# Kernel tuning notes

Measured on AMD Instinct MI355X. Metric: run time of the kernel, lower is better.

The kernel has to match this reference:

```python
import jax, jax.numpy as jnp
import numpy as np

IMG, P, CIN, D, K, L, H, FF, B = 512, 32, 3, 256, 8192, 6, 8, 1024, 32
GRID = IMG // P  # 16
DH = D // H
EPS = 1e-5


def _ln(x, w, b):
    m = x.mean(-1, keepdims=True)
    v = ((x - m) ** 2).mean(-1, keepdims=True)
    return (x - m) / jnp.sqrt(v + EPS) * w + b


def _mha(x, wqkv, bqkv, wo, bo):
    # x: (S, Bt, D) -- axis 0 is the attention axis (torch batch_first=False quirk)
    S, Bt, _ = x.shape
    qkv = x @ wqkv.T + bqkv
    q, k, v = jnp.split(qkv, 3, axis=-1)
    q = q.reshape(S, Bt, H, DH)
    k = k.reshape(S, Bt, H, DH)
    v = v.reshape(S, Bt, H, DH)
    scores = jnp.einsum('sbhd,tbhd->bhst', q, k) / jnp.sqrt(jnp.float32(DH))
    attn = jax.nn.softmax(scores, axis=-1)
    o = jnp.einsum('bhst,tbhd->sbhd', attn, v).reshape(S, Bt, D)
    return o @ wo.T + bo


def _conv_t(x, w, b, stride=2, pad=1):
    # w uses torch ConvTranspose2d layout (Cin, Cout, kH, kW)
    kH = w.shape[2]
    wf = jnp.flip(w, (2, 3)).transpose(1, 0, 2, 3)  # -> (Cout, Cin, kH, kW)
    y = jax.lax.conv_general_dilated(
        x, wf, window_strides=(1, 1),
        padding=[(kH - 1 - pad, kH - 1 - pad)] * 2,
        lhs_dilation=(stride, stride),
        dimension_numbers=('NCHW', 'OIHW', 'NCHW'))
    return y + b[None, :, None, None]


def _forward(x, patch_w, patch_b, qkv_w, qkv_b, out_w, out_b, ln1_w, ln1_b,
             ln2_w, ln2_b, ff1_w, ff1_b, ff2_w, ff2_b, lnf_w, lnf_b, codebook,
             dec_w0, dec_b0, dec_w1, dec_b1, dec_w2, dec_b2, dec_w3, dec_b3):
    # patch embedding: conv stride=patch -> (B, D, G, G) -> (B, N, D)
    h = jax.lax.conv_general_dilated(
        x, patch_w, (P, P), 'VALID',
        dimension_numbers=('NCHW', 'OIHW', 'NCHW')) + patch_b[None, :, None, None]
    h = h.reshape(h.shape[0], D, -1).transpose(0, 2, 1)  # (B, N, D)
    # torch TransformerEncoderLayer default batch_first=False: attention runs
    # over axis 0 (image batch); faithfully replicated here. Post-norm, eval
    # mode (dropout=identity), exact gelu.
    for i in range(L):
        a = _mha(h, qkv_w[i], qkv_b[i], out_w[i], out_b[i])
        h = _ln(h + a, ln1_w[i], ln1_b[i])
        f = jax.nn.gelu(h @ ff1_w[i].T + ff1_b[i], approximate=False) @ ff2_w[i].T + ff2_b[i]
        h = _ln(h + f, ln2_w[i], ln2_b[i])
    h = _ln(h, lnf_w, lnf_b)
    # vector quantization: squared-distance argmin over codebook
    flat = h.reshape(-1, D)  # (B*N, D)
    d = ((flat ** 2).sum(-1, keepdims=True)
         - 2.0 * flat @ codebook.T
         + (codebook ** 2).sum(-1))  # (B*N, K)
    idx = jnp.argmin(d, axis=1)
    q = codebook[idx].reshape(h.shape)
    e_loss = jnp.mean((jax.lax.stop_gradient(q) - h) ** 2)
    q_loss = jnp.mean((q - jax.lax.stop_gradient(h)) ** 2)
    vq_loss = q_loss + 0.25 * e_loss
    q = h + jax.lax.stop_gradient(q - h)  # straight-through
    q = q.transpose(0, 2, 1).reshape(x.shape[0], D, GRID, GRID)
    y = jax.nn.relu(_conv_t(q, dec_w0, dec_b0))
    y = jax.nn.relu(_conv_t(y, dec_w1, dec_b1))
    y = jax.nn.relu(_conv_t(y, dec_w2, dec_b2))
    x_hat = jax.nn.sigmoid(_conv_t(y, dec_w3, dec_b3))
    return x_hat, vq_loss


def setup_inputs() -> dict:
    key = jax.random.key(0)
    ks = iter(jax.random.split(key, 64))
    nrm = lambda shape, s=0.02: jax.random.normal(next(ks), shape, jnp.float32) * s
    f32 = jnp.float32
    return {
        'x': jax.random.normal(next(ks), (B, CIN, IMG, IMG), f32),
        'patch_w': nrm((D, CIN, P, P)),
        'patch_b': jnp.zeros((D,), f32),
        'qkv_w': nrm((L, 3 * D, D)),
        'qkv_b': jnp.zeros((L, 3 * D), f32),
        'out_w': nrm((L, D, D)),
        'out_b': jnp.zeros((L, D), f32),
        'ln1_w': jnp.ones((L, D), f32),
        'ln1_b': jnp.zeros((L, D), f32),
        'ln2_w': jnp.ones((L, D), f32),
        'ln2_b': jnp.zeros((L, D), f32),
        'ff1_w': nrm((L, FF, D)),
        'ff1_b': jnp.zeros((L, FF), f32),
        'ff2_w': nrm((L, D, FF)),
        'ff2_b': jnp.zeros((L, D), f32),
        'lnf_w': jnp.ones((D,), f32),
        'lnf_b': jnp.zeros((D,), f32),
        'codebook': jax.random.uniform(next(ks), (K, D), f32, -1.0 / K, 1.0 / K),
        'dec_w0': nrm((D, 256, 4, 4)),
        'dec_b0': jnp.zeros((256,), f32),
        'dec_w1': nrm((256, 128, 4, 4)),
        'dec_b1': jnp.zeros((128,), f32),
        'dec_w2': nrm((128, 64, 4, 4)),
        'dec_b2': jnp.zeros((64,), f32),
        'dec_w3': nrm((64, CIN, 4, 4)),
        'dec_b3': jnp.zeros((CIN,), f32),
    }


def reference(x, patch_w, patch_b, qkv_w, qkv_b, out_w, out_b, ln1_w, ln1_b,
              ln2_w, ln2_b, ff1_w, ff1_b, ff2_w, ff2_b, lnf_w, lnf_b, codebook,
              dec_w0, dec_b0, dec_w1, dec_b1, dec_w2, dec_b2, dec_w3, dec_b3):
    return _forward(x, patch_w, patch_b, qkv_w, qkv_b, out_w, out_b, ln1_w,
                    ln1_b, ln2_w, ln2_b, ff1_w, ff1_b, ff2_w, ff2_b, lnf_w,
                    lnf_b, codebook, dec_w0, dec_b0, dec_w1, dec_b1, dec_w2,
                    dec_b2, dec_w3, dec_b3)
```

## Files before the change

### kernel.cpp

```cpp
#include <hip/hip_runtime.h>
#include <hip/hip_bf16.h>
#include <math.h>

typedef __hip_bfloat16 bf16;
typedef unsigned int u32;
typedef unsigned long long u64;
using short8 = __attribute__((ext_vector_type(8))) short;
using f32x4  = __attribute__((ext_vector_type(4))) float;

__device__ __forceinline__ float b2f(bf16 v){ return __bfloat162float(v); }
__device__ __forceinline__ bf16  f2b(float v){ return __float2bfloat16(v); }
__device__ __forceinline__ float plo(u32 u){ return __uint_as_float(u << 16); }
__device__ __forceinline__ float phi(u32 u){ return __uint_as_float(u & 0xffff0000u); }

__device__ __forceinline__ void gld16(const void* g, void* l)
{
  __builtin_amdgcn_global_load_lds(
      (const __attribute__((address_space(1))) u32*)g,
      (__attribute__((address_space(3))) u32*)l, 16, 0, 0);
}

__global__ void k_detect(const u32* probe, int* flag)
{
  if (threadIdx.x == 0 && blockIdx.x == 0)
    *flag = (*probe == 0x3F800000u) ? 0 : 1;
}

struct PPack { const void* s[25]; u32 off[26]; };
__global__ __launch_bounds__(256) void k_convall(PPack pp, bf16* P, const int* flag)
{
  const u32 i = blockIdx.x * 256 + threadIdx.x;
  if (i >= pp.off[25]) return;
  int lo = 0, hi = 25;
  while (hi - lo > 1) { const int mid = (lo + hi) >> 1; if (i >= pp.off[mid]) lo = mid; else hi = mid; }
  const u32 j = i - pp.off[lo];
  P[i] = *flag ? ((const bf16*)pp.s[lo])[j] : f2b(((const float*)pp.s[lo])[j]);
}

__global__ __launch_bounds__(256) void k_zborder(bf16* buf, int Hp, int C, int nimg)
{
  const int per = 4 * Hp - 4;
  const int c8 = C >> 3;
  const int total = nimg * per * c8;
  const int i = blockIdx.x * 256 + threadIdx.x;
  if (i >= total) return;
  const int ch8 = i % c8;
  const int pb = i / c8;
  const int img = pb / per;
  const int b = pb - img * per;
  int y, x;
  if (b < Hp) { y = 0; x = b; }
  else if (b < 2 * Hp) { y = Hp - 1; x = b - Hp; }
  else {
    const int r = b - 2 * Hp;
    const int side = r / (Hp - 2);
    y = 1 + r - side * (Hp - 2);
    x = side ? (Hp - 1) : 0;
  }
  uint4 z = {0, 0, 0, 0};
  *reinterpret_cast<uint4*>(buf + (((size_t)img * Hp + y) * Hp + x) * C + ch8 * 8) = z;
}

__global__ __launch_bounds__(128) void k_im2col(const void* x, bf16* A, const int* flag)
{
  const int m = blockIdx.y;
  const int k8 = blockIdx.x * 128 + threadIdx.x;
  const int k = k8 * 8;
  const int b = m >> 8, n = m & 255;
  const int gy = n >> 4, gx = n & 15;
  const int c = k >> 10, r = (k >> 5) & 31, pp = k & 31;
  const size_t src = (((size_t)(b * 3 + c) * 512) + gy * 32 + r) * 512 + gx * 32 + pp;
  bf16 ov[8];
  if (*flag) {
    const bf16* xp = (const bf16*)x + src;
    #pragma unroll
    for (int i = 0; i < 8; ++i) ov[i] = xp[i];
  } else {
    const float4 v0 = *reinterpret_cast<const float4*>((const float*)x + src);
    const float4 v1 = *reinterpret_cast<const float4*>((const float*)x + src + 4);
    ov[0]=f2b(v0.x); ov[1]=f2b(v0.y); ov[2]=f2b(v0.z); ov[3]=f2b(v0.w);
    ov[4]=f2b(v1.x); ov[5]=f2b(v1.y); ov[6]=f2b(v1.z); ov[7]=f2b(v1.w);
  }
  *reinterpret_cast<uint4*>(A + (size_t)m * 3072 + k) = *reinterpret_cast<const uint4*>(ov);
}

template<int EPI, int FM, int BN, bool DB>
__global__ __launch_bounds__(256, 2) void gemm_t(
    const bf16* __restrict__ A, const bf16* __restrict__ Bw,
    const bf16* __restrict__ bias, const bf16* res, bf16* C,
    const float* __restrict__ cnorm, u64* __restrict__ ku,
    int M, int N, int K, int Kc)
{
  constexpr int BM = FM * 32;
  constexpr int FN = BN / 32;
  __shared__ alignas(16) bf16 As[DB ? 2 : 1][BM * 64];
  __shared__ alignas(16) bf16 Bs[DB ? 2 : 1][BN * 64];
  const int tid = threadIdx.x;
  const int bn = blockIdx.x * BN, bm = blockIdx.y * BM;
  const int z = blockIdx.z;
  const int kb = z * Kc;
  const int l = tid & 63, w = tid >> 6;
  const int wm = w >> 1, wn = w & 1;
  const int lg = l >> 4, lr = l & 15;
  const int sr8 = l >> 3;
  const int sch = (l & 7) ^ sr8;
  f32x4 acc[FM][FN];
  #pragma unroll
  for (int fm = 0; fm < FM; ++fm)
    #pragma unroll
    for (int fn = 0; fn < FN; ++fn) acc[fm][fn] = (f32x4){0.f, 0.f, 0.f, 0.f};

  auto stage = [&](int bb, int k0) {
    char* ab = (char*)As[bb];
    char* bp = (char*)Bs[bb];
    #pragma unroll
    for (int it = 0; it < FM; ++it) {
      const int r = w * 8 + it * 32 + sr8;
      gld16(A + (size_t)(bm + r) * K + k0 + sch * 8, ab + w * 1024 + it * 4096);
    }
    #pragma unroll
    for (int it = 0; it < BN / 32; ++it) {
      const int r = w * 8 + it * 32 + sr8;
      gld16(Bw + (size_t)(bn + r) * K + k0 + sch * 8, bp + w * 1024 + it * 4096);
    }
  };
  auto compute = [&](int bb) {
    const char* ab = (const char*)As[bb];
    const char* bp = (const char*)Bs[bb];
    #pragma unroll
    for (int ks = 0; ks < 2; ++ks) {
      short8 af[FM], bfr[FN];
      #pragma unroll
      for (int fm = 0; fm < FM; ++fm) {
        const int r = wm * (FM * 16) + fm * 16 + lr;
        af[fm] = *reinterpret_cast<const short8*>(ab + r * 128 + (((lg + ks * 4) ^ (r & 7)) * 16));
      }
      #pragma unroll
      for (int fn = 0; fn < FN; ++fn) {
        const int r = wn * (BN / 2) + fn * 16 + lr;
        bfr[fn] = *reinterpret_cast<const short8*>(bp + r * 128 + (((lg + ks * 4) ^ (r & 7)) * 16));
      }
      #pragma unroll
      for (int fm = 0; fm < FM; ++fm)
        #pragma unroll
        for (int fn = 0; fn < FN; ++fn)
          acc[fm][fn] = __builtin_amdgcn_mfma_f32_16x16x32_bf16(af[fm], bfr[fn], acc[fm][fn], 0, 0, 0);
    }
  };

  const int nt = Kc >> 6;
  if (DB) {
    stage(0, kb);
    __syncthreads();
    for (int t = 0; t < nt; ++t) {
      const int cur = t & 1;
      if (t + 1 < nt) stage(cur ^ 1, kb + ((t + 1) << 6));
      compute(cur);
      __syncthreads();
    }
  } else {
    for (int t = 0; t < nt; ++t) {
      if (t) __syncthreads();
      stage(0, kb + (t << 6));
      __syncthreads();
      compute(0);
    }
  }

  if (EPI == 3) {
    __shared__ u64 skey[BM][2];
    float cn[FN];
    #pragma unroll
    for (int fn = 0; fn < FN; ++fn) cn[fn] = cnorm[bn + wn * (BN / 2) + fn * 16 + lr];
    #pragma unroll
    for (int fm = 0; fm < FM; ++fm) {
      #pragma unroll
      for (int r = 0; r < 4; ++r) {
        u64 best = ~0ull;
        #pragma unroll
        for (int fn = 0; fn < FN; ++fn) {
          const int col = bn + wn * (BN / 2) + fn * 16 + lr;
          const float d = cn[fn] - 2.0f * acc[fm][fn][r];
          u32 u = __float_as_uint(d);
          u = (u & 0x80000000u) ? ~u : (u | 0x80000000u);
          const u64 key = ((u64)u << 32) | (u32)col;
          best = key < best ? key : best;
        }
        #pragma unroll
        for (int mk = 1; mk < 16; mk <<= 1) {
          const u64 o = __shfl_xor(best, mk, 64);
          best = o < best ? o : best;
        }
        if (lr == 0) skey[wm * (FM * 16) + fm * 16 + lg * 4 + r][wn] = best;
      }
    }
    __syncthreads();
    if (tid < BM) {
      const u64 a = skey[tid][0], b = skey[tid][1];
      ku[(size_t)blockIdx.x * M + bm + tid] = a < b ? a : b;
    }
  } else if (EPI == 4) {
    #pragma unroll
    for (int fm = 0; fm < FM; ++fm) {
      const int m0 = bm + wm * (FM * 16) + fm * 16 + lg * 4;
      #pragma unroll
      for (int fn = 0; fn < FN; ++fn) {
        const int n = bn + wn * (BN / 2) + fn * 16 + lr;
        #pragma unroll
        for (int r = 0; r < 4; ++r)
          C[((size_t)z * M + m0 + r) * N + n] = f2b(acc[fm][fn][r]);
      }
    }
  } else {
    #pragma unroll
    for (int fm = 0; fm < FM; ++fm) {
      const int m0 = bm + wm * (FM * 16) + fm * 16 + lg * 4;
      #pragma unroll
      for (int fn = 0; fn < FN; ++fn) {
        const int n = bn + wn * (BN / 2) + fn * 16 + lr;
        const float bs = b2f(bias[n]);
        #pragma unroll
        for (int r = 0; r < 4; ++r) {
          float v = acc[fm][fn][r] + bs;
          if (EPI == 1) v = 0.5f * v * (1.0f + erff(v * 0.70710678118654752f));
          if (EPI == 2) v += b2f(res[(size_t)(m0 + r) * N + n]);
          C[(size_t)(m0 + r) * N + n] = f2b(v);
        }
      }
    }
  }
}

__global__ __launch_bounds__(256, 1) void k_fat1(
    bf16* __restrict__ hbuf,
    const bf16* __restrict__ Wqkv, const bf16* __restrict__ Bqkv,
    const bf16* __restrict__ Wo, const bf16* __restrict__ Bo,
    const bf16* __restrict__ lw, const bf16* __restrict__ lb)
{
  __shared__ alignas(16) bf16 hs[32 * 256];
  __shared__ alignas(16) bf16 ao[32 * 256];
  __shared__ alignas(16) bf16 astage[128 * 64];
  __shared__ bf16 att[3 * 9216];
  __shared__ float ps[32][33];
  __shared__ float rs[32];
  __shared__ float psum[32][4], psq[32][4];
  __shared__ float mstat[32], istat[32];

  const int bt = blockIdx.x;
  const int tid = threadIdx.x;
  const int l = tid & 63, w = tid >> 6;
  const int lg = l >> 4, lr = l & 15;
  const int sr8 = l >> 3;
  const int sch = (l & 7) ^ sr8;
  char* hsb = (char*)hs;
  char* aob = (char*)ao;
  char* asb = (char*)astage;

  #pragma unroll
  for (int call = 0; call < 4; ++call) {
    const int id = call * 256 + tid;
    const int s = id >> 5, within = id & 31;
    const int grp = within >> 3, c = within & 7;
    gld16(hbuf + (size_t)(s * 256 + bt) * 256 + grp * 64 + ((c ^ (s & 7)) * 8),
          hsb + call * 4096 + w * 1024);
  }

  for (int at = 0; at < 6; ++at) {
    f32x4 acc[2][2];
    #pragma unroll
    for (int fm = 0; fm < 2; ++fm)
      #pragma unroll
      for (int fn = 0; fn < 2; ++fn) acc[fm][fn] = (f32x4){0.f, 0.f, 0.f, 0.f};
    for (int kst = 0; kst < 4; ++kst) {
      __syncthreads();
      #pragma unroll
      for (int it = 0; it < 4; ++it) {
        const int r = w * 8 + it * 32 + sr8;
        gld16(Wqkv + (size_t)(at * 128 + r) * 256 + kst * 64 + sch * 8,
              asb + w * 1024 + it * 4096);
      }
      __syncthreads();
      #pragma unroll
      for (int ks = 0; ks < 2; ++ks) {
        short8 af[2], bfr[2];
        #pragma unroll
        for (int fm = 0; fm < 2; ++fm) {
          const int r = w * 32 + fm * 16 + lr;
          af[fm] = *reinterpret_cast<const short8*>(asb + r * 128 + (((lg + ks * 4) ^ (r & 7)) * 16));
        }
        #pragma unroll
        for (int fn = 0; fn < 2; ++fn) {
          const int sr = fn * 16 + lr;
          bfr[fn] = *reinterpret_cast<const short8*>(hsb + sr * 512 + kst * 128 + (((lg + ks * 4) ^ (sr & 7)) * 16));
        }
        #pragma unroll
        for (int fm = 0; fm < 2; ++fm)
          #pragma unroll
          for (int fn = 0; fn < 2; ++fn)
            acc[fm][fn] = __builtin_amdgcn_mfma_f32_16x16x32_bf16(af[fm], bfr[fn], acc[fm][fn], 0, 0, 0);
      }
    }
    #pragma unroll
    for (int fm = 0; fm < 2; ++fm) {
      #pragma unroll
      for (int fn = 0; fn < 2; ++fn) {
        const int s = fn * 16 + lr;
        #pragma unroll
        for (int r = 0; r < 4; ++r) {
          const int n = at * 128 + w * 32 + fm * 16 + lg * 4 + r;
          const int p = n >> 8, rem = n & 255;
          att[p * 9216 + (rem >> 5) * 1152 + s * 36 + (rem & 31)] =
              f2b(acc[fm][fn][r] + b2f(Bqkv[n]));
        }
      }
    }
  }
  __syncthreads();

  const int s_a = tid >> 3, j_a = tid & 7;
  for (int hd = 0; hd < 8; ++hd) {
    const bf16* qrow = att + hd * 1152 + s_a * 36;
    float sc[4];
    #pragma unroll
    for (int e = 0; e < 4; ++e) {
      const int t = j_a + 8 * e;
      const bf16* krow = att + 9216 + hd * 1152 + t * 36;
      float v = 0.f;
      #pragma unroll
      for (int dd = 0; dd < 32; ++dd) v += b2f(qrow[dd]) * b2f(krow[dd]);
      sc[e] = v * 0.17677669529663687f;
    }
    float mx = fmaxf(fmaxf(sc[0], sc[1]), fmaxf(sc[2], sc[3]));
    #pragma unroll
    for (int mk = 1; mk < 8; mk <<= 1) mx = fmaxf(mx, __shfl_xor(mx, mk, 64));
    float sm = 0.f; float ex[4];
    #pragma unroll
    for (int e = 0; e < 4; ++e) { ex[e] = expf(sc[e] - mx); sm += ex[e]; }
    #pragma unroll
    for (int mk = 1; mk < 8; mk <<= 1) sm += __shfl_xor(sm, mk, 64);
    #pragma unroll
    for (int e = 0; e < 4; ++e) ps[s_a][j_a + 8 * e] = ex[e];
    if (j_a == 0) rs[s_a] = 1.0f / sm;
    __syncthreads();
    const float rinv = rs[s_a];
    float av[4];
    #pragma unroll
    for (int e = 0; e < 4; ++e) {
      const int dd = j_a * 4 + e;
      float a = 0.f;
      #pragma unroll
      for (int t = 0; t < 32; ++t)
        a += ps[s_a][t] * b2f(att[2 * 9216 + hd * 1152 + t * 36 + dd]);
      av[e] = a * rinv;
    }
    alignas(8) bf16 ov[4];
    #pragma unroll
    for (int e = 0; e < 4; ++e) ov[e] = f2b(av[e]);
    const int clog = (hd & 1) * 4 + (j_a >> 1);
    *reinterpret_cast<ushort4*>(aob + s_a * 512 + (hd >> 1) * 128 +
        ((clog ^ (s_a & 7)) * 16) + (j_a & 1) * 8) =
        *reinterpret_cast<const ushort4*>(ov);
    __syncthreads();
  }

  float vals[2][2][2][4];
  for (int at = 0; at < 2; ++at) {
    f32x4 acc[2][2];
    #pragma unroll
    for (int fm = 0; fm < 2; ++fm)
      #pragma unroll
      for (int fn = 0; fn < 2; ++fn) acc[fm][fn] = (f32x4){0.f, 0.f, 0.f, 0.f};
    for (int kst = 0; kst < 4; ++kst) {
      __syncthreads();
      #pragma unroll
      for (int it = 0; it < 4; ++it) {
        const int r = w * 8 + it * 32 + sr8;
        gld16(Wo + (size_t)(at * 128 + r) * 256 + kst * 64 + sch * 8,
              asb + w * 1024 + it * 4096);
      }
      __syncthreads();
      #pragma unroll
      for (int ks = 0; ks < 2; ++ks) {
        short8 af[2], bfr[2];
        #pragma unroll
        for (int fm = 0; fm < 2; ++fm) {
          const int r = w * 32 + fm * 16 + lr;
          af[fm] = *reinterpret_cast<const short8*>(asb + r * 128 + (((lg + ks * 4) ^ (r & 7)) * 16));
        }
        #pragma unroll
        for (int fn = 0; fn < 2; ++fn) {
          const int sr = fn * 16 + lr;
          bfr[fn] = *reinterpret_cast<const short8*>(aob + sr * 512 + kst * 128 + (((lg + ks * 4) ^ (sr & 7)) * 16));
        }
        #pragma unroll
        for (int fm = 0; fm < 2; ++fm)
          #pragma unroll
          for (int fn = 0; fn < 2; ++fn)
            acc[fm][fn] = __builtin_amdgcn_mfma_f32_16x16x32_bf16(af[fm], bfr[fn], acc[fm][fn], 0, 0, 0);
      }
    }
    #pragma unroll
    for (int fm = 0; fm < 2; ++fm)
      #pragma unroll
      for (int fn = 0; fn < 2; ++fn)
        #pragma unroll
        for (int r = 0; r < 4; ++r) vals[at][fm][fn][r] = acc[fm][fn][r];
  }

  float s1[2] = {0.f, 0.f}, s2[2] = {0.f, 0.f};
  #pragma unroll
  for (int at = 0; at < 2; ++at) {
    #pragma unroll
    for (int fm = 0; fm < 2; ++fm) {
      const int n4 = at * 128 + w * 32 + fm * 16 + lg * 4;
      #pragma unroll
      for (int fn = 0; fn < 2; ++fn) {
        const int s = fn * 16 + lr;
        const ushort4 hr = *reinterpret_cast<const ushort4*>(
            hsb + s * 512 + (n4 >> 6) * 128 + ((((n4 >> 3) & 7) ^ (s & 7)) * 16) + (n4 & 7) * 2);
        const bf16* hb = reinterpret_cast<const bf16*>(&hr);
        #pragma unroll
        for (int r = 0; r < 4; ++r) {
          const float v = vals[at][fm][fn][r] + b2f(Bo[n4 + r]) + b2f(hb[r]);
          vals[at][fm][fn][r] = v;
          s1[fn] += v;
          s2[fn] += v * v;
        }
      }
    }
  }
  #pragma unroll
  for (int fn = 0; fn < 2; ++fn) {
    float a = s1[fn], b = s2[fn];
    a += __shfl_xor(a, 16, 64); a += __shfl_xor(a, 32, 64);
    b += __shfl_xor(b, 16, 64); b += __shfl_xor(b, 32, 64);
    if (lg == 0) { psum[fn * 16 + lr][w] = a; psq[fn * 16 + lr][w] = b; }
  }
  __syncthreads();
  if (tid < 32) {
    float sa = 0.f, sb = 0.f;
    #pragma unroll
    for (int k = 0; k < 4; ++k) { sa += psum[tid][k]; sb += psq[tid][k]; }
    const float m = sa * (1.0f / 256.0f);
    mstat[tid] = m;
    istat[tid] = 1.0f / sqrtf(sb * (1.0f / 256.0f) - m * m + 1e-5f);
  }
  __syncthreads();
  #pragma unroll
  for (int at = 0; at < 2; ++at) {
    #pragma unroll
    for (int fm = 0; fm < 2; ++fm) {
      const int n4 = at * 128 + w * 32 + fm * 16 + lg * 4;
      #pragma unroll
      for (int fn = 0; fn < 2; ++fn) {
        const int s = fn * 16 + lr;
        const float m = mstat[s], inv = istat[s];
        alignas(8) bf16 ov[4];
        #pragma unroll
        for (int r = 0; r < 4; ++r)
          ov[r] = f2b((vals[at][fm][fn][r] - m) * inv * b2f(lw[n4 + r]) + b2f(lb[n4 + r]));
        *reinterpret_cast<ushort4*>(hbuf + (size_t)(s * 256 + bt) * 256 + n4) =
            *reinterpret_cast<const ushort4*>(ov);
      }
    }
  }
}

template<bool DOLN>
__global__ __launch_bounds__(256) void k_lnred(
    const bf16* __restrict__ Pf, const bf16* __restrict__ bias,
    const bf16* res, const bf16* __restrict__ lw, const bf16* __restrict__ lb,
    const bf16* lw2, const bf16* lb2,
    bf16* h, int kc)
{
  __shared__ float wsum[4], wsq[4];
  const int row = blockIdx.x, d = threadIdx.x;
  const int w = d >> 6;
  float s = 0.f;
  for (int z = 0; z < kc; ++z) s += b2f(Pf[((size_t)z * 8192 + row) * 256 + d]);
  s += b2f(bias[d]);
  if (res) s += b2f(res[(size_t)row * 256 + d]);
  if (!DOLN) { h[(size_t)row * 256 + d] = f2b(s); return; }
  float a = s, b = s * s;
  #pragma unroll
  for (int mk = 1; mk < 64; mk <<= 1) {
    a += __shfl_xor(a, mk, 64);
    b += __shfl_xor(b, mk, 64);
  }
  if ((d & 63) == 0) { wsum[w] = a; wsq[w] = b; }
  __syncthreads();
  float sa = wsum[0] + wsum[1] + wsum[2] + wsum[3];
  float sb = wsq[0] + wsq[1] + wsq[2] + wsq[3];
  float m = sa * (1.0f / 256.0f);
  float inv = 1.0f / sqrtf(sb * (1.0f / 256.0f) - m * m + 1e-5f);
  float y = (s - m) * inv * b2f(lw[d]) + b2f(lb[d]);
  if (lw2) {
    __syncthreads();
    a = y; b = y * y;
    #pragma unroll
    for (int mk = 1; mk < 64; mk <<= 1) {
      a += __shfl_xor(a, mk, 64);
      b += __shfl_xor(b, mk, 64);
    }
    if ((d & 63) == 0) { wsum[w] = a; wsq[w] = b; }
    __syncthreads();
    sa = wsum[0] + wsum[1] + wsum[2] + wsum[3];
    sb = wsq[0] + wsq[1] + wsq[2] + wsq[3];
    m = sa * (1.0f / 256.0f);
    inv = 1.0f / sqrtf(sb * (1.0f / 256.0f) - m * m + 1e-5f);
    y = (y - m) * inv * b2f(lw2[d]) + b2f(lb2[d]);
  }
  h[(size_t)row * 256 + d] = f2b(y);
}

__global__ __launch_bounds__(256) void k_vqmerge(
    const u64* __restrict__ ku, int* __restrict__ idx, int M, int NB)
{
  const int r = blockIdx.x * 256 + threadIdx.x;
  if (r >= M) return;
  u64 best = ku[r];
  for (int nb = 1; nb < NB; ++nb) {
    const u64 k = ku[(size_t)nb * M + r];
    best = k < best ? k : best;
  }
  idx[r] = (int)(best & 0xFFFFFFFFull);
}

__global__ __launch_bounds__(256) void k_cnorm(const bf16* __restrict__ cb, float* __restrict__ cn)
{
  const int j = blockIdx.x * 256 + threadIdx.x;
  const u32* p = (const u32*)(cb + (size_t)j * 256);
  float s = 0.f;
  for (int k = 0; k < 128; ++k) {
    const u32 v = p[k];
    const float a = plo(v), b = phi(v);
    s += a * a + b * b;
  }
  cn[j] = s;
}

__global__ __launch_bounds__(256) void k_gather(
    const bf16* h, const bf16* cb, const int* idx, bf16* a0, float* lsum)
{
  __shared__ float ws[4];
  const int row = blockIdx.x, d = threadIdx.x;
  const int w = d >> 6;
  const int code = idx[row] & 8191;
  const float q = b2f(cb[(size_t)code * 256 + d]);
  const float x = b2f(h[(size_t)row * 256 + d]);
  float v = (q - x) * (q - x);
  #pragma unroll
  for (int mk = 1; mk < 64; mk <<= 1) v += __shfl_xor(v, mk, 64);
  if ((d & 63) == 0) ws[w] = v;
  __syncthreads();
  if (d == 0) lsum[row] = ws[0] + ws[1] + ws[2] + ws[3];
  const int b = row >> 8, n = row & 255;
  const int y = n >> 4, xc = n & 15;
  a0[(((size_t)b * 18 + y + 1) * 18 + (xc + 1)) * 256 + d] = f2b(q);
}

__global__ __launch_bounds__(256) void k_loss(const float* lsum, float* out)
{
  __shared__ float red[256];
  const int tid = threadIdx.x;
  float v = 0.f;
  for (int i = 0; i < 32; ++i) v += lsum[tid + 256 * i];
  red[tid] = v;
  __syncthreads();
  for (int off = 128; off > 0; off >>= 1) {
    if (tid < off) red[tid] += red[tid + off];
    __syncthreads();
  }
  if (tid == 0)
    out[0] = red[0] * (1.25f / 2097152.0f);
}

__global__ __launch_bounds__(256) void k_wtrans(
    const bf16* __restrict__ w, bf16* __restrict__ wt,
    int Cin, int lCin, int CoutR, int CoutP)
{
  const int K = Cin << 2;
  const int total = 4 * CoutP * K;
  const int i = blockIdx.x * 256 + threadIdx.x;
  if (i >= total) return;
  const int p = i / (CoutP * K);
  const int rem = i - p * (CoutP * K);
  const int co = rem / K;
  const int k = rem - co * K;
  const int tap = k >> lCin, ci = k - (tap << lCin);
  const int py = p >> 1, px = p & 1, ty = tap >> 1, tx = tap & 1;
  bf16 v = f2b(0.f);
  if (co < CoutR)
    v = w[(((size_t)ci * CoutR + co) * 4 + py + 2 * ty) * 4 + px + 2 * tx];
  wt[i] = v;
}

__global__ __launch_bounds__(256, 2) void convt64(
    const bf16* __restrict__ in, const bf16* __restrict__ Wt,
    const bf16* __restrict__ bias, bf16* __restrict__ outp,
    int H, int lH, int Cin, int lCin, int Cout)
{
  __shared__ alignas(16) bf16 As[2][128 * 64];
  __shared__ alignas(16) bf16 Bs[2][64 * 64];
  const int tid = threadIdx.x;
  const int pz = blockIdx.z;
  const int py = pz >> 1, px = pz & 1;
  const int K = Cin << 2;
  const int bn = blockIdx.x * 64, bm = blockIdx.y * 128;
  const bf16* Bw = Wt + (size_t)pz * Cout * K;
  const int l = tid & 63, w = tid >> 6;
  const int wm = w >> 1, wn = w & 1;
  const int lg = l >> 4, lr = l & 15;
  const int sr8 = l >> 3;
  const int sch = (l & 7) ^ sr8;
  const int Hp = H + 2;
  f32x4 acc[4][2];
  #pragma unroll
  for (int fm = 0; fm < 4; ++fm)
    #pragma unroll
    for (int fn = 0; fn < 2; ++fn) acc[fm][fn] = (f32x4){0.f, 0.f, 0.f, 0.f};

  size_t pixbase[4];
  #pragma unroll
  for (int it = 0; it < 4; ++it) {
    const int m = bm + w * 8 + it * 32 + sr8;
    const int b = m >> (2 * lH);
    const int rem = m & ((1 << (2 * lH)) - 1);
    const int jj = rem >> lH, ii = rem & (H - 1);
    pixbase[it] = ((size_t)(b * Hp + jj) * Hp + ii);
  }

  auto stage = [&](int bb, int k0) {
    char* ab = (char*)As[bb];
    char* bp = (char*)Bs[bb];
    const int tap = k0 >> lCin;
    const int ty = tap >> 1, tx = tap & 1;
    const int sy = (1 - py) + (1 - ty);
    const int sx = (1 - px) + (1 - tx);
    const int ci0 = (k0 - (tap << lCin)) + sch * 8;
    #pragma unroll
    for (int it = 0; it < 4; ++it)
      gld16(in + (pixbase[it] + (size_t)sy * Hp + sx) * Cin + ci0,
            ab + w * 1024 + it * 4096);
    #pragma unroll
    for (int it = 0; it < 2; ++it) {
      const int r = w * 8 + it * 32 + sr8;
      gld16(Bw + (size_t)(bn + r) * K + k0 + sch * 8, bp + w * 1024 + it * 4096);
    }
  };

  const int nt = K >> 6;
  stage(0, 0);
  __syncthreads();
  for (int t = 0; t < nt; ++t) {
    const int cur = t & 1;
    if (t + 1 < nt) stage(cur ^ 1, (t + 1) << 6);
    const char* ab = (const char*)As[cur];
    const char* bb = (const char*)Bs[cur];
    #pragma unroll
    for (int ks = 0; ks < 2; ++ks) {
      short8 af[4], bfr[2];
      #pragma unroll
      for (int fm = 0; fm < 4; ++fm) {
        const int r = wm * 64 + fm * 16 + lr;
        af[fm] = *reinterpret_cast<const short8*>(ab + r * 128 + (((lg + ks * 4) ^ (r & 7)) * 16));
      }
      #pragma unroll
      for (int fn = 0; fn < 2; ++fn) {
        const int r = wn * 32 + fn * 16 + lr;
        bfr[fn] = *reinterpret_cast<const short8*>(bb + r * 128 + (((lg + ks * 4) ^ (r & 7)) * 16));
      }
      #pragma unroll
      for (int fm = 0; fm < 4; ++fm)
        #pragma unroll
        for (int fn = 0; fn < 2; ++fn)
          acc[fm][fn] = __builtin_amdgcn_mfma_f32_16x16x32_bf16(af[fm], bfr[fn], acc[fm][fn], 0, 0, 0);
    }
    __syncthreads();
  }

  const int Ho = 2 * H, Hop = Ho + 2;
  #pragma unroll
  for (int fm = 0; fm < 4; ++fm) {
    const int m0 = bm + wm * 64 + fm * 16 + lg * 4;
    #pragma unroll
    for (int fn = 0; fn < 2; ++fn) {
      const int n = bn + wn * 32 + fn * 16 + lr;
      #pragma unroll
      for (int r = 0; r < 4; ++r) {
        const int m = m0 + r;
        const int b = m >> (2 * lH);
        const int rem = m & ((1 << (2 * lH)) - 1);
        const int jj = rem >> lH, ii = rem & (H - 1);
        const int oy = 2 * jj + (1 - py), ox = 2 * ii + (1 - px);
        const float v = fmaxf(acc[fm][fn][r] + b2f(bias[n]), 0.f);
        outp[((size_t)(b * Hop + oy + 1) * Hop + ox + 1) * Cout + n] = f2b(v);
      }
    }
  }
}

__global__ __launch_bounds__(256) void k_dec3(
    const bf16* __restrict__ a3, const bf16* __restrict__ wt3,
    const bf16* __restrict__ bias, float* __restrict__ xhat, int chunkBase)
{
  __shared__ float wl[3][264];
  const int tid = threadIdx.x;
  const int pz = blockIdx.y;
  const int py = pz >> 1, px = pz & 1;
  for (int i = tid; i < 768; i += 256) {
    const int co = i >> 8, k = i & 255;
    wl[co][k] = b2f(wt3[(pz * 3 + co) * 256 + k]);
  }
  __syncthreads();
  const int b = blockIdx.z;
  const int p = blockIdx.x * 64 + (tid >> 2);
  const int jj = p >> 7, ii = p & 127;
  const int ch4 = tid & 3;
  float a0 = 0.f, a1 = 0.f, a2 = 0.f;
  #pragma unroll
  for (int ty = 0; ty < 2; ++ty) {
    #pragma unroll
    for (int tx = 0; tx < 2; ++tx) {
      const int sy = (1 - py) + (1 - ty), sx = (1 - px) + (1 - tx);
      const int tap = ty * 2 + tx;
      const u32* ip = (const u32*)(a3 + ((size_t)(b * 130 + jj + sy) * 130 + ii + sx) * 64) + ch4 * 8;
      const float* w0 = &wl[0][tap * 64 + ch4 * 16];
      const float* w1 = &wl[1][tap * 64 + ch4 * 16];
      const float* w2 = &wl[2][tap * 64 + ch4 * 16];
      #pragma unroll
      for (int kk = 0; kk < 8; ++kk) {
        const u32 v = ip[kk];
        const float e0 = plo(v), e1 = phi(v);
        a0 += e0 * w0[2 * kk] + e1 * w0[2 * kk + 1];
        a1 += e0 * w1[2 * kk] + e1 * w1[2 * kk + 1];
        a2 += e0 * w2[2 * kk] + e1 * w2[2 * kk + 1];
      }
    }
  }
  a0 += __shfl_xor(a0, 1, 64); a0 += __shfl_xor(a0, 2, 64);
  a1 += __shfl_xor(a1, 1, 64); a1 += __shfl_xor(a1, 2, 64);
  a2 += __shfl_xor(a2, 1, 64); a2 += __shfl_xor(a2, 2, 64);
  if (ch4 < 3) {
    const float av = ch4 == 0 ? a0 : (ch4 == 1 ? a1 : a2);
    const int oy = 2 * jj + (1 - py), ox = 2 * ii + (1 - px);
    const float t = av + b2f(bias[ch4]);
    xhat[(((size_t)(chunkBase + b) * 3 + ch4) * 256 + oy) * 256 + ox] =
        1.0f / (1.0f + expf(-t));
  }
}

extern "C" void kernel_launch(void* const* d_in, const int* in_sizes, int n_in,
                              void* d_out, int out_size, void* d_ws, size_t ws_size,
                              hipStream_t stream)
{
  float* xhat = (float*)d_out;
  float* lossout = xhat + (out_size - 1);

  const size_t NEED = 130195456;
  if (ws_size < NEED) return;

  char* ws = (char*)d_ws;
  int*   flag  = (int*)  (ws + 0);
  float* lsum  = (float*)(ws + 1024);
  int*   idx   = (int*)  (ws + 65536);
  u64*   ku    = (u64*)  (ws + 131072);
  bf16*  P     = (bf16*) (ws + 8519680);
  bf16*  WT    = (bf16*) (ws + 27262976);
  float* cnorm = (float*)(ws + 30900224);
  bf16*  hbuf  = (bf16*) (ws + 31457280);
  bf16*  A_im  = (bf16*) (ws + 35651584);
  bf16*  ffb   = (bf16*) (ws + 52428800);
  bf16*  Pfb   = (bf16*) (ws + 85983232);
  bf16*  a0    = (bf16*) (ws + 35651584);
  bf16*  a1    = (bf16*) (ws + 40960000);
  bf16*  a2    = (bf16*) (ws + 59899904);
  bf16*  a3    = (bf16*) (ws + 95584256);

  k_detect<<<1, 64, 0, stream>>>((const u32*)d_in[7], flag);

  size_t poff[26]; poff[1] = 0;
  for (int i = 2; i <= 25; ++i) poff[i] = poff[i - 1] + (size_t)in_sizes[i - 1];
  const size_t ptotal = poff[25] + (size_t)in_sizes[25];
  PPack pp;
  for (int i = 0; i < 25; ++i) { pp.s[i] = d_in[i + 1]; pp.off[i] = (u32)poff[i + 1]; }
  pp.off[25] = (u32)ptotal;
  k_convall<<<(int)((ptotal + 255) / 256), 256, 0, stream>>>(pp, P, flag);

  const bf16 *patch_w = P + poff[1],  *patch_b = P + poff[2];
  const bf16 *qkv_w   = P + poff[3],  *qkv_b   = P + poff[4];
  const bf16 *out_w   = P + poff[5],  *out_b   = P + poff[6];
  const bf16 *ln1_w   = P + poff[7],  *ln1_b   = P + poff[8];
  const bf16 *ln2_w   = P + poff[9],  *ln2_b   = P + poff[10];
  const bf16 *ff1_w   = P + poff[11], *ff1_b   = P + poff[12];
  const bf16 *ff2_w   = P + poff[13], *ff2_b   = P + poff[14];
  const bf16 *lnf_w   = P + poff[15], *lnf_b   = P + poff[16];
  const bf16 *codebook= P + poff[17];
  const bf16 *dec_w0  = P + poff[18], *dec_b0  = P + poff[19];
  const bf16 *dec_w1  = P + poff[20], *dec_b1  = P + poff[21];
  const bf16 *dec_w2  = P + poff[22], *dec_b2  = P + poff[23];
  const bf16 *dec_w3  = P + poff[24], *dec_b3  = P + poff[25];

  bf16* wt0 = WT;
  bf16* wt1 = wt0 + 1048576;
  bf16* wt2 = wt1 + 524288;
  bf16* wt3 = wt2 + 131072;
  k_wtrans<<<(1048576 + 255) / 256, 256, 0, stream>>>(dec_w0, wt0, 256, 8, 256, 256);
  k_wtrans<<<(524288 + 255) / 256, 256, 0, stream>>>(dec_w1, wt1, 256, 8, 128, 128);
  k_wtrans<<<(131072 + 255) / 256, 256, 0, stream>>>(dec_w2, wt2, 128, 7, 64, 64);
  k_wtrans<<<(3072 + 255) / 256, 256, 0, stream>>>(dec_w3, wt3, 64, 6, 3, 3);
  k_cnorm<<<32, 256, 0, stream>>>(codebook, cnorm);

  k_im2col<<<dim3(3, 8192), 128, 0, stream>>>(d_in[0], A_im, flag);
  gemm_t<4, 2, 128, true><<<dim3(2, 128, 4), 256, 0, stream>>>(
      A_im, patch_w, nullptr, nullptr, Pfb, nullptr, nullptr, 8192, 256, 3072, 768);
  k_lnred<false><<<8192, 256, 0, stream>>>(
      Pfb, patch_b, nullptr, nullptr, nullptr, nullptr, nullptr, hbuf, 4);

  for (int l = 0; l < 6; ++l) {
    k_fat1<<<256, 256, 0, stream>>>(
        hbuf, qkv_w + (size_t)l * 768 * 256, qkv_b + l * 768,
        out_w + (size_t)l * 256 * 256, out_b + l * 256,
        ln1_w + l * 256, ln1_b + l * 256);
    gemm_t<1, 2, 256, false><<<dim3(4, 128, 1), 256, 0, stream>>>(
        hbuf, ff1_w + (size_t)l * 1024 * 256, ff1_b + l * 1024, nullptr, ffb,
        nullptr, nullptr, 8192, 1024, 256, 256);
    gemm_t<4, 2, 128, false><<<dim3(2, 128, 2), 256, 0, stream>>>(
        ffb, ff2_w + (size_t)l * 256 * 1024, nullptr, nullptr, Pfb,
        nullptr, nullptr, 8192, 256, 1024, 512);
    k_lnred<true><<<8192, 256, 0, stream>>>(
        Pfb, ff2_b + l * 256, hbuf, ln2_w + l * 256, ln2_b + l * 256,
        (l == 5) ? lnf_w : nullptr, (l == 5) ? lnf_b : nullptr, hbuf, 2);
  }

  gemm_t<3, 2, 256, false><<<dim3(32, 128, 1), 256, 0, stream>>>(
      hbuf, codebook, nullptr, nullptr, nullptr, cnorm, ku, 8192, 8192, 256, 256);
  k_vqmerge<<<32, 256, 0, stream>>>(ku, idx, 8192, 32);

  k_zborder<<<(32 * 68 * 32 + 255) / 256, 256, 0, stream>>>(a0, 18, 256, 32);
  k_gather<<<8192, 256, 0, stream>>>(hbuf, codebook, idx, a0, lsum);
  k_loss<<<1, 256, 0, stream>>>(lsum, lossout);
  k_zborder<<<(32 * 132 * 32 + 255) / 256, 256, 0, stream>>>(a1, 34, 256, 32);
  k_zborder<<<(32 * 260 * 16 + 255) / 256, 256, 0, stream>>>(a2, 66, 128, 32);
  k_zborder<<<(16 * 516 * 8 + 255) / 256, 256, 0, stream>>>(a3, 130, 64, 16);

  convt64<<<dim3(4, 64, 4), 256, 0, stream>>>(a0, wt0, dec_b0, a1, 16, 4, 256, 8, 256);
  convt64<<<dim3(2, 256, 4), 256, 0, stream>>>(a1, wt1, dec_b1, a2, 32, 5, 256, 8, 128);
  for (int c = 0; c < 2; ++c) {
    const bf16* a2c = a2 + (size_t)c * 16 * 66 * 66 * 128;
    convt64<<<dim3(1, 512, 4), 256, 0, stream>>>(a2c, wt2, dec_b2, a3, 64, 6, 128, 7, 64);
    k_dec3<<<dim3(256, 4, 16), 256, 0, stream>>>(a3, wt3, dec_b3, xhat, c * 16);
  }
}
```

Measured before the change: 927.7 us.

## Add dedicated VQ distance-argmin kernel with full-K LDS staging and 128x128 tiles

Replaces the generic GEMM template used for the codebook distance and argmin with a dedicated kernel. It loads the whole K=256 slice of 128 rows of activations and 128 codes into swizzled LDS in one go, runs MFMA, then reduces packed (distance,index) keys within the block. The grid changes to 64x64 tiles, so the merge kernel now sees 64 partial candidates per row instead of 32. It uses 128KB of LDS per block, which limits occupancy to one block per CU and leaves no overlap between loads and compute.

```diff
diff --git a/kernel.cpp b/kernel.cpp
--- a/kernel.cpp
+++ b/kernel.cpp
@@ -231,6 +231,99 @@
   }
 }
 
+__global__ __launch_bounds__(256, 1) void k_vq(
+    const bf16* __restrict__ A, const bf16* __restrict__ Bw,
+    const float* __restrict__ cnorm, u64* __restrict__ ku, int M)
+{
+  __shared__ alignas(16) bf16 As[4 * 128 * 64];
+  __shared__ alignas(16) bf16 Bs[4 * 128 * 64];
+  __shared__ u64 skey[128][2];
+  const int tid = threadIdx.x;
+  const int bn = blockIdx.x * 128, bm = blockIdx.y * 128;
+  const int l = tid & 63, w = tid >> 6;
+  const int wm = w >> 1, wn = w & 1;
+  const int lg = l >> 4, lr = l & 15;
+  const int sr8 = l >> 3;
+  const int sch = (l & 7) ^ sr8;
+  char* asb = (char*)As;
+  char* bsb = (char*)Bs;
+
+  #pragma unroll
+  for (int c = 0; c < 4; ++c) {
+    #pragma unroll
+    for (int it = 0; it < 4; ++it) {
+      const int r = w * 8 + it * 32 + sr8;
+      gld16(A + (size_t)(bm + r) * 256 + c * 64 + sch * 8,
+            asb + c * 16384 + w * 1024 + it * 4096);
+      gld16(Bw + (size_t)(bn + r) * 256 + c * 64 + sch * 8,
+            bsb + c * 16384 + w * 1024 + it * 4096);
+    }
+  }
+  __syncthreads();
+
+  f32x4 acc[4][4];
+  #pragma unroll
+  for (int fm = 0; fm < 4; ++fm)
+    #pragma unroll
+    for (int fn = 0; fn < 4; ++fn) acc[fm][fn] = (f32x4){0.f, 0.f, 0.f, 0.f};
+
+  #pragma unroll
+  for (int kst = 0; kst < 4; ++kst) {
+    const char* ab = asb + kst * 16384;
+    const char* bp = bsb + kst * 16384;
+    #pragma unroll
+    for (int ks = 0; ks < 2; ++ks) {
+      short8 af[4], bfr[4];
+      #pragma unroll
+      for (int fm = 0; fm < 4; ++fm) {
+        const int r = wm * 64 + fm * 16 + lr;
+        af[fm] = *reinterpret_cast<const short8*>(ab + r * 128 + (((lg + ks * 4) ^ (r & 7)) * 16));
+      }
+      #pragma unroll
+      for (int fn = 0; fn < 4; ++fn) {
+        const int r = wn * 64 + fn * 16 + lr;
+        bfr[fn] = *reinterpret_cast<const short8*>(bp + r * 128 + (((lg + ks * 4) ^ (r & 7)) * 16));
+      }
+      #pragma unroll
+      for (int fm = 0; fm < 4; ++fm)
+        #pragma unroll
+        for (int fn = 0; fn < 4; ++fn)
+          acc[fm][fn] = __builtin_amdgcn_mfma_f32_16x16x32_bf16(af[fm], bfr[fn], acc[fm][fn], 0, 0, 0);
+    }
+  }
+
+  float cn[4];
+  #pragma unroll
+  for (int fn = 0; fn < 4; ++fn) cn[fn] = cnorm[bn + wn * 64 + fn * 16 + lr];
+  #pragma unroll
+  for (int fm = 0; fm < 4; ++fm) {
+    #pragma unroll
+    for (int r = 0; r < 4; ++r) {
+      u64 best = ~0ull;
+      #pragma unroll
+      for (int fn = 0; fn < 4; ++fn) {
+        const int col = bn + wn * 64 + fn * 16 + lr;
+        const float d = cn[fn] - 2.0f * acc[fm][fn][r];
+        u32 u = __float_as_uint(d);
+        u = (u & 0x80000000u) ? ~u : (u | 0x80000000u);
+        const u64 key = ((u64)u << 32) | (u32)col;
+        best = key < best ? key : best;
+      }
+      #pragma unroll
+      for (int mk = 1; mk < 16; mk <<= 1) {
+        const u64 o = __shfl_xor(best, mk, 64);
+        best = o < best ? o : best;
+      }
+      if (lr == 0) skey[wm * 64 + fm * 16 + lg * 4 + r][wn] = best;
+    }
+  }
+  __syncthreads();
+  if (tid < 128) {
+    const u64 a = skey[tid][0], b = skey[tid][1];
+    ku[(size_t)blockIdx.x * M + bm + tid] = a < b ? a : b;
+  }
+}
+
 __global__ __launch_bounds__(256, 1) void k_fat1(
     bf16* __restrict__ hbuf,
     const bf16* __restrict__ Wqkv, const bf16* __restrict__ Bqkv,
@@ -833,9 +926,8 @@
         (l == 5) ? lnf_w : nullptr, (l == 5) ? lnf_b : nullptr, hbuf, 2);
   }
 
-  gemm_t<3, 2, 256, false><<<dim3(32, 128, 1), 256, 0, stream>>>(
-      hbuf, codebook, nullptr, nullptr, nullptr, cnorm, ku, 8192, 8192, 256, 256);
-  k_vqmerge<<<32, 256, 0, stream>>>(ku, idx, 8192, 32);
+  k_vq<<<dim3(64, 64), 256, 0, stream>>>(hbuf, codebook, cnorm, ku, 8192);
+  k_vqmerge<<<32, 256, 0, stream>>>(ku, idx, 8192, 64);
 
   k_zborder<<<(32 * 68 * 32 + 255) / 256, 256, 0, stream>>>(a0, 18, 256, 32);
   k_gather<<<8192, 256, 0, stream>>>(hbuf, codebook, idx, a0, lsum);
```

Measured after the change: 1.012 ms. +9.1%, slower.
